# Kernel tuning notes

Measured on AMD Instinct MI355X. Metric: run time of the kernel, lower is better.

Reference implementation:

```python
import jax, jax.numpy as jnp
import numpy as np

N_RAY = 65536
K = 256
NX = NY = NZ = 256


def setup_inputs() -> dict:
    key = jax.random.key(0)
    k1, k2, k3 = jax.random.split(key, 3)
    volume = jax.random.uniform(k1, (NX, NY, NZ), dtype=jnp.float32)
    M = jnp.eye(3, dtype=jnp.float32)          # voxel spacing 1, axis-aligned
    b = jnp.zeros(3, dtype=jnp.float32)        # origin at voxel (0,0,0)
    # rays travel along +z through the volume; random (x, y) entry points
    xy = jax.random.uniform(k2, (N_RAY, 2), minval=0.0, maxval=float(NX - 1), dtype=jnp.float32)
    src = jnp.concatenate([xy, jnp.full((N_RAY, 1), -1.0, dtype=jnp.float32)], axis=1)
    dst = jnp.concatenate([xy, jnp.full((N_RAY, 1), float(NZ), dtype=jnp.float32)], axis=1)
    # sorted sampling parameters t in [0, 1] per ray (uncompressed t_sorted branch)
    t_sorted = jnp.sort(jax.random.uniform(k3, (N_RAY, K), dtype=jnp.float32), axis=1)
    return {"volume": volume, "M": M, "b": b, "src": src, "dst": dst, "t_sorted": t_sorted}


def reference(volume, M, b, src, dst, t_sorted):
    """Faithful jax port of forward_project_3d_torch (uncompressed, fully vectorized)."""
    nx, ny, nz = volume.shape
    M_inv = jnp.linalg.inv(M)
    # sample points along each ray: [N, K, 3]
    direc = (dst - src)[:, None, :]
    pts = src[:, None, :] + t_sorted[:, :, None] * direc
    p0 = pts[:, :-1, :]   # segment starts [N, K-1, 3]
    p1 = pts[:, 1:, :]    # segment ends   [N, K-1, 3]
    inf_mask = jnp.any(jnp.isinf(p0) | jnp.isinf(p1), axis=-1)
    seg_len = jnp.sqrt(jnp.sum((p1 - p0) ** 2, axis=-1))          # [N, K-1]
    mid = 0.5 * (p0 + p1) - b                                      # shifted midpoints
    # voxel-space coordinates: M_inv @ mid, per segment
    ijk_f = jnp.einsum('rc,nkc->nkr', M_inv, mid)                  # [N, K-1, 3]
    ijk = jnp.round(ijk_f).astype(jnp.int32)
    i_idx, j_idx, k_idx = ijk[..., 0], ijk[..., 1], ijk[..., 2]
    oob = (i_idx < 0) | (i_idx >= nx) | (j_idx < 0) | (j_idx >= ny) | (k_idx < 0) | (k_idx >= nz)
    valid = (~inf_mask) & (~oob)
    flat_idx = jnp.where(valid, i_idx * (ny * nz) + j_idx * nz + k_idx, 0)
    vox = volume.reshape(-1)[flat_idx]                             # gather [N, K-1]
    seg_val = jnp.where(valid, vox * seg_len, jnp.zeros_like(seg_len))
    return jnp.sum(seg_val, axis=1)                                # sinogram [N]
```

## Files before the change

kernel.cpp:

```cpp
#include <hip/hip_runtime.h>
#include <math.h>

#define N_RAY 65536
#define KPTS 256
#define NXV 256
#define NYV 256
#define NZV 256
#define RPW 8

typedef float f4vec __attribute__((ext_vector_type(4)));

__global__ __launch_bounds__(256, 4) void ct_proj_kernel(
    const float* __restrict__ volume,
    const float* __restrict__ Mmat,
    const float* __restrict__ bvec,
    const float* __restrict__ src,
    const float* __restrict__ dst,
    const float* __restrict__ t_sorted,
    float* __restrict__ out)
{
    __shared__ float rowbuf[4][2][NZV];

    const int lane = threadIdx.x & 63;
    const int wid  = threadIdx.x >> 6;
    const int wave = blockIdx.x * 4 + wid;
    const int ray0 = wave * RPW;

    float (* __restrict__ slice)[NZV] = rowbuf[wid];

    const int sdi = lane < 24 ? lane : 23;
    const float sv = src[3 * ray0 + sdi];
    const float dv = dst[3 * ray0 + sdi];

    const float* tbase = t_sorted + (size_t)ray0 * KPTS;
    f4vec tvv[RPW];
    #pragma unroll
    for (int i = 0; i < 4; ++i)
        tvv[i] = __builtin_nontemporal_load(
            reinterpret_cast<const f4vec*>(tbase + i * KPTS + 4 * lane));

    const float bx = bvec[0], by = bvec[1], bz = bvec[2];
    const bool fastM =
        (Mmat[0] == 1.0f) && (Mmat[1] == 0.0f) && (Mmat[2] == 0.0f) &&
        (Mmat[3] == 0.0f) && (Mmat[4] == 1.0f) && (Mmat[5] == 0.0f) &&
        (Mmat[6] == 0.0f) && (Mmat[7] == 0.0f) && (Mmat[8] == 1.0f) &&
        (bx == 0.0f) && (by == 0.0f) && (bz == 0.0f);

    unsigned fmask = 0u, imask = 0u;
    unsigned RO[RPW];
    #pragma unroll
    for (int i = 0; i < RPW; ++i) {
        const float sx = __shfl(sv, 3 * i + 0, 64);
        const float sy = __shfl(sv, 3 * i + 1, 64);
        const float sz = __shfl(sv, 3 * i + 2, 64);
        const float dxv = __fsub_rn(__shfl(dv, 3 * i + 0, 64), sx);
        const float dyv = __fsub_rn(__shfl(dv, 3 * i + 1, 64), sy);
        const float dzv = __fsub_rn(__shfl(dv, 3 * i + 2, 64), sz);
        const bool fr = fastM && (dxv == 0.0f) && (dyv == 0.0f) &&
                        isfinite(sx) && isfinite(sy) && isfinite(sz) &&
                        isfinite(dzv);
        const int ii = (int)rintf(sx);
        const int jj = (int)rintf(sy);
        const bool inb = ((unsigned)ii < NXV) && ((unsigned)jj < NYV);
        fmask |= (fr  ? 1u : 0u) << i;
        imask |= (inb ? 1u : 0u) << i;
        RO[i] = __builtin_amdgcn_readfirstlane(
            (fr && inb) ? ((unsigned)ii * NYV + (unsigned)jj) * NZV : 0u);
    }
    fmask = __builtin_amdgcn_readfirstlane(fmask);
    imask = __builtin_amdgcn_readfirstlane(imask);

    const unsigned vo = 4u * (unsigned)lane;
    f4vec rvv[RPW];
    #pragma unroll
    for (int i = 0; i < 3; ++i)
        rvv[i] = *reinterpret_cast<const f4vec*>(volume + RO[i] + vo);

    #define WRITE_SLICE(s, r) do {                 \
        slice[s][0 * 64 + lane] = (r).x;           \
        slice[s][1 * 64 + lane] = (r).y;           \
        slice[s][2 * 64 + lane] = (r).z;           \
        slice[s][3 * 64 + lane] = (r).w;           \
    } while (0)

    WRITE_SLICE(0, rvv[0]);

    #pragma unroll
    for (int i = 0; i < RPW; ++i) {
        if (i + 1 < RPW) WRITE_SLICE((i + 1) & 1, rvv[i + 1]);
        if (i + 3 < RPW)
            rvv[i + 3] = *reinterpret_cast<const f4vec*>(volume + RO[i + 3] + vo);
        if (i + 4 < RPW)
            tvv[i + 4] = __builtin_nontemporal_load(
                reinterpret_cast<const f4vec*>(tbase + (i + 4) * KPTS + 4 * lane));

        const int ray = ray0 + i;
        float acc = 0.0f;

        if ((fmask >> i) & 1u) {
            if ((imask >> i) & 1u) {
                const float sz  = __shfl(sv, 3 * i + 2, 64);
                const float dzv = __fsub_rn(__shfl(dv, 3 * i + 2, 64), sz);
                const f4vec tv  = tvv[i];
                const float t4  = __shfl_down(tv.x, 1, 64);
                const float* __restrict__ buf = slice[i & 1];

                const float p0 = __fadd_rn(sz, __fmul_rn(tv.x, dzv));
                const float p1 = __fadd_rn(sz, __fmul_rn(tv.y, dzv));
                const float p2 = __fadd_rn(sz, __fmul_rn(tv.z, dzv));
                const float p3 = __fadd_rn(sz, __fmul_rn(tv.w, dzv));
                const float p4 = __fadd_rn(sz, __fmul_rn(t4,   dzv));

                const bool f0 = !isinf(p0), f1 = !isinf(p1), f2 = !isinf(p2),
                           f3 = !isinf(p3), f4 = !isinf(p4);

                {
                    const float ez   = __fsub_rn(p1, p0);
                    const float midz = __fmul_rn(0.5f, __fadd_rn(p0, p1));
                    const int   kk   = (int)rintf(midz);
                    const bool  v    = ((unsigned)kk < NZV) && f0 && f1;
                    const int   a    = ((kk & 3) << 6) + (kk >> 2);
                    acc = fmaf(buf[v ? a : 0], v ? fabsf(ez) : 0.0f, acc);
                }
                {
                    const float ez   = __fsub_rn(p2, p1);
                    const float midz = __fmul_rn(0.5f, __fadd_rn(p1, p2));
                    const int   kk   = (int)rintf(midz);
                    const bool  v    = ((unsigned)kk < NZV) && f1 && f2;
                    const int   a    = ((kk & 3) << 6) + (kk >> 2);
                    acc = fmaf(buf[v ? a : 0], v ? fabsf(ez) : 0.0f, acc);
                }
                {
                    const float ez   = __fsub_rn(p3, p2);
                    const float midz = __fmul_rn(0.5f, __fadd_rn(p2, p3));
                    const int   kk   = (int)rintf(midz);
                    const bool  v    = ((unsigned)kk < NZV) && f2 && f3;
                    const int   a    = ((kk & 3) << 6) + (kk >> 2);
                    acc = fmaf(buf[v ? a : 0], v ? fabsf(ez) : 0.0f, acc);
                }
                {
                    const float ez   = __fsub_rn(p4, p3);
                    const float midz = __fmul_rn(0.5f, __fadd_rn(p3, p4));
                    const int   kk   = (int)rintf(midz);
                    const bool  v    = ((unsigned)kk < NZV) && f3 && f4 &&
                                       (lane != 63);
                    const int   a    = ((kk & 3) << 6) + (kk >> 2);
                    acc = fmaf(buf[v ? a : 0], v ? fabsf(ez) : 0.0f, acc);
                }
            }
        } else {
            const float sx = __shfl(sv, 3 * i + 0, 64);
            const float sy = __shfl(sv, 3 * i + 1, 64);
            const float sz = __shfl(sv, 3 * i + 2, 64);
            const float dxv = __fsub_rn(__shfl(dv, 3 * i + 0, 64), sx);
            const float dyv = __fsub_rn(__shfl(dv, 3 * i + 1, 64), sy);
            const float dzv = __fsub_rn(__shfl(dv, 3 * i + 2, 64), sz);

            const float m00 = Mmat[0], m01 = Mmat[1], m02 = Mmat[2];
            const float m10 = Mmat[3], m11 = Mmat[4], m12 = Mmat[5];
            const float m20 = Mmat[6], m21 = Mmat[7], m22 = Mmat[8];
            const float c00 =  (m11 * m22 - m12 * m21);
            const float c01 = -(m10 * m22 - m12 * m20);
            const float c02 =  (m10 * m21 - m11 * m20);
            const float det = m00 * c00 + m01 * c01 + m02 * c02;
            const float id  = 1.0f / det;
            const float i00 = c00 * id;
            const float i01 = -(m01 * m22 - m02 * m21) * id;
            const float i02 =  (m01 * m12 - m02 * m11) * id;
            const float i10 = c01 * id;
            const float i11 =  (m00 * m22 - m02 * m20) * id;
            const float i12 = -(m00 * m12 - m02 * m10) * id;
            const float i20 = c02 * id;
            const float i21 = -(m00 * m21 - m01 * m20) * id;
            const float i22 =  (m00 * m11 - m01 * m10) * id;

            const float* t = tbase + i * KPTS;
            #pragma unroll
            for (int it = 0; it < 4; ++it) {
                const int idx = it * 64 + lane;
                if (idx < KPTS - 1) {
                    const float tkv  = t[idx];
                    const float tk1v = t[idx + 1];
                    const float p0x = __fadd_rn(sx, __fmul_rn(tkv,  dxv));
                    const float p0y = __fadd_rn(sy, __fmul_rn(tkv,  dyv));
                    const float p0z = __fadd_rn(sz, __fmul_rn(tkv,  dzv));
                    const float p1x = __fadd_rn(sx, __fmul_rn(tk1v, dxv));
                    const float p1y = __fadd_rn(sy, __fmul_rn(tk1v, dyv));
                    const float p1z = __fadd_rn(sz, __fmul_rn(tk1v, dzv));

                    const bool infm = isinf(p0x) || isinf(p0y) || isinf(p0z) ||
                                      isinf(p1x) || isinf(p1y) || isinf(p1z);

                    const float ex = __fsub_rn(p1x, p0x);
                    const float ey = __fsub_rn(p1y, p0y);
                    const float ez = __fsub_rn(p1z, p0z);
                    const float seg = sqrtf(ex * ex + ey * ey + ez * ez);

                    const float mx = __fsub_rn(__fmul_rn(0.5f, __fadd_rn(p0x, p1x)), bx);
                    const float my = __fsub_rn(__fmul_rn(0.5f, __fadd_rn(p0y, p1y)), by);
                    const float mz = __fsub_rn(__fmul_rn(0.5f, __fadd_rn(p0z, p1z)), bz);

                    const float fi = __fadd_rn(__fadd_rn(__fmul_rn(i00, mx), __fmul_rn(i01, my)), __fmul_rn(i02, mz));
                    const float fj = __fadd_rn(__fadd_rn(__fmul_rn(i10, mx), __fmul_rn(i11, my)), __fmul_rn(i12, mz));
                    const float fk = __fadd_rn(__fadd_rn(__fmul_rn(i20, mx), __fmul_rn(i21, my)), __fmul_rn(i22, mz));

                    const int ii = (int)rintf(fi);
                    const int jj = (int)rintf(fj);
                    const int kk = (int)rintf(fk);

                    const bool oob = (ii < 0) || (ii >= NXV) ||
                                     (jj < 0) || (jj >= NYV) ||
                                     (kk < 0) || (kk >= NZV);

                    if (!infm && !oob) {
                        const float vox = volume[((size_t)ii * NYV + jj) * NZV + kk];
                        acc = fmaf(vox, seg, acc);
                    }
                }
            }
        }

        #pragma unroll
        for (int off = 32; off >= 1; off >>= 1)
            acc += __shfl_xor(acc, off, 64);

        if (lane == 0) out[ray] = acc;
    }
    #undef WRITE_SLICE
}

extern "C" void kernel_launch(void* const* d_in, const int* in_sizes, int n_in,
                              void* d_out, int out_size, void* d_ws, size_t ws_size,
                              hipStream_t stream) {
    const float* volume   = (const float*)d_in[0];
    const float* Mmat     = (const float*)d_in[1];
    const float* bvec     = (const float*)d_in[2];
    const float* src      = (const float*)d_in[3];
    const float* dst      = (const float*)d_in[4];
    const float* t_sorted = (const float*)d_in[5];
    float* out = (float*)d_out;

    const int grid = N_RAY / (RPW * 4);
    ct_proj_kernel<<<grid, 256, 0, stream>>>(volume, Mmat, bvec, src, dst,
                                             t_sorted, out);
}
```

Measured before the change: 152.5 us.

## Stream t-values and volume rows into LDS via global_load_lds with a 4-slot pipeline

Replaces register-held prefetches plus manual LDS writes with direct global-to-LDS DMA loads (global_load_lds) for both the t_sorted rows and the volume z-rows. A 4-slot ring per wave keeps three rays in flight, synchronised with explicit vmcnt/lgkmcnt waits. It also drops the swizzled LDS layout in favour of linear indexing, writes all 8 ray outputs with one coalesced store, and hoists the M inverse out of the slow-path loop. The intent is to cut VGPR pressure and LDS write instructions and to improve latency hiding. The cost is reliance on hand-tuned waitcnt counts, removal of the min-occupancy launch bound, and possible LDS bank conflicts from the linear layout.

```diff
diff --git a/kernel.cpp b/kernel.cpp
--- a/kernel.cpp
+++ b/kernel.cpp
@@ -10,7 +10,15 @@
 
 typedef float f4vec __attribute__((ext_vector_type(4)));
 
-__global__ __launch_bounds__(256, 4) void ct_proj_kernel(
+#define GLDS16(gsrc, ldst)                                                \
+    __builtin_amdgcn_global_load_lds(                                     \
+        (const __attribute__((address_space(1))) void*)(gsrc),            \
+        (__attribute__((address_space(3))) void*)(ldst), 16, 0, 0)
+
+#define WAITVM(n)  asm volatile("s_waitcnt vmcnt(" #n ")" ::: "memory")
+#define WAITLGKM0  asm volatile("s_waitcnt lgkmcnt(0)" ::: "memory")
+
+__global__ __launch_bounds__(256) void ct_proj_kernel(
     const float* __restrict__ volume,
     const float* __restrict__ Mmat,
     const float* __restrict__ bvec,
@@ -19,25 +27,16 @@
     const float* __restrict__ t_sorted,
     float* __restrict__ out)
 {
-    __shared__ float rowbuf[4][2][NZV];
+    __shared__ float tslot[4][4][KPTS];
+    __shared__ float rslot[4][4][NZV];
 
     const int lane = threadIdx.x & 63;
     const int wid  = threadIdx.x >> 6;
-    const int wave = blockIdx.x * 4 + wid;
-    const int ray0 = wave * RPW;
-
-    float (* __restrict__ slice)[NZV] = rowbuf[wid];
+    const int ray0 = (blockIdx.x * 4 + wid) * RPW;
 
     const int sdi = lane < 24 ? lane : 23;
     const float sv = src[3 * ray0 + sdi];
     const float dv = dst[3 * ray0 + sdi];
-
-    const float* tbase = t_sorted + (size_t)ray0 * KPTS;
-    f4vec tvv[RPW];
-    #pragma unroll
-    for (int i = 0; i < 4; ++i)
-        tvv[i] = __builtin_nontemporal_load(
-            reinterpret_cast<const f4vec*>(tbase + i * KPTS + 4 * lane));
 
     const float bx = bvec[0], by = bvec[1], bz = bvec[2];
     const bool fastM =
@@ -70,85 +69,110 @@
     fmask = __builtin_amdgcn_readfirstlane(fmask);
     imask = __builtin_amdgcn_readfirstlane(imask);
 
-    const unsigned vo = 4u * (unsigned)lane;
-    f4vec rvv[RPW];
-    #pragma unroll
-    for (int i = 0; i < 3; ++i)
-        rvv[i] = *reinterpret_cast<const f4vec*>(volume + RO[i] + vo);
-
-    #define WRITE_SLICE(s, r) do {                 \
-        slice[s][0 * 64 + lane] = (r).x;           \
-        slice[s][1 * 64 + lane] = (r).y;           \
-        slice[s][2 * 64 + lane] = (r).z;           \
-        slice[s][3 * 64 + lane] = (r).w;           \
-    } while (0)
-
-    WRITE_SLICE(0, rvv[0]);
-
-    #pragma unroll
-    for (int i = 0; i < RPW; ++i) {
-        if (i + 1 < RPW) WRITE_SLICE((i + 1) & 1, rvv[i + 1]);
-        if (i + 3 < RPW)
-            rvv[i + 3] = *reinterpret_cast<const f4vec*>(volume + RO[i + 3] + vo);
-        if (i + 4 < RPW)
-            tvv[i + 4] = __builtin_nontemporal_load(
-                reinterpret_cast<const f4vec*>(tbase + (i + 4) * KPTS + 4 * lane));
-
-        const int ray = ray0 + i;
-        float acc = 0.0f;
-
-        if ((fmask >> i) & 1u) {
-            if ((imask >> i) & 1u) {
-                const float sz  = __shfl(sv, 3 * i + 2, 64);
-                const float dzv = __fsub_rn(__shfl(dv, 3 * i + 2, 64), sz);
-                const f4vec tv  = tvv[i];
-                const float t4  = __shfl_down(tv.x, 1, 64);
-                const float* __restrict__ buf = slice[i & 1];
-
-                const float p0 = __fadd_rn(sz, __fmul_rn(tv.x, dzv));
-                const float p1 = __fadd_rn(sz, __fmul_rn(tv.y, dzv));
-                const float p2 = __fadd_rn(sz, __fmul_rn(tv.z, dzv));
-                const float p3 = __fadd_rn(sz, __fmul_rn(tv.w, dzv));
-                const float p4 = __fadd_rn(sz, __fmul_rn(t4,   dzv));
-
-                const bool f0 = !isinf(p0), f1 = !isinf(p1), f2 = !isinf(p2),
-                           f3 = !isinf(p3), f4 = !isinf(p4);
-
-                {
-                    const float ez   = __fsub_rn(p1, p0);
-                    const float midz = __fmul_rn(0.5f, __fadd_rn(p0, p1));
-                    const int   kk   = (int)rintf(midz);
-                    const bool  v    = ((unsigned)kk < NZV) && f0 && f1;
-                    const int   a    = ((kk & 3) << 6) + (kk >> 2);
-                    acc = fmaf(buf[v ? a : 0], v ? fabsf(ez) : 0.0f, acc);
-                }
-                {
-                    const float ez   = __fsub_rn(p2, p1);
-                    const float midz = __fmul_rn(0.5f, __fadd_rn(p1, p2));
-                    const int   kk   = (int)rintf(midz);
-                    const bool  v    = ((unsigned)kk < NZV) && f1 && f2;
-                    const int   a    = ((kk & 3) << 6) + (kk >> 2);
-                    acc = fmaf(buf[v ? a : 0], v ? fabsf(ez) : 0.0f, acc);
-                }
-                {
-                    const float ez   = __fsub_rn(p3, p2);
-                    const float midz = __fmul_rn(0.5f, __fadd_rn(p2, p3));
-                    const int   kk   = (int)rintf(midz);
-                    const bool  v    = ((unsigned)kk < NZV) && f2 && f3;
-                    const int   a    = ((kk & 3) << 6) + (kk >> 2);
-                    acc = fmaf(buf[v ? a : 0], v ? fabsf(ez) : 0.0f, acc);
-                }
-                {
-                    const float ez   = __fsub_rn(p4, p3);
-                    const float midz = __fmul_rn(0.5f, __fadd_rn(p3, p4));
-                    const int   kk   = (int)rintf(midz);
-                    const bool  v    = ((unsigned)kk < NZV) && f3 && f4 &&
-                                       (lane != 63);
-                    const int   a    = ((kk & 3) << 6) + (kk >> 2);
-                    acc = fmaf(buf[v ? a : 0], v ? fabsf(ez) : 0.0f, acc);
-                }
-            }
-        } else {
+    const float* tbase = t_sorted + (size_t)ray0 * KPTS;
+    float rsel = 0.0f;
+
+    if (fmask == 0xFFu) {
+        WAITVM(0);
+
+        #pragma unroll
+        for (int i = 0; i < 3; ++i) {
+            GLDS16(tbase + i * KPTS + 4 * lane, &tslot[wid][i][0]);
+            GLDS16(volume + RO[i] + 4 * lane,   &rslot[wid][i][0]);
+        }
+
+        #pragma unroll
+        for (int i = 0; i < RPW; ++i) {
+            if (i < 5) {
+                WAITLGKM0;
+                GLDS16(tbase + (i + 3) * KPTS + 4 * lane,
+                       &tslot[wid][(i + 3) & 3][0]);
+                GLDS16(volume + RO[i + 3] + 4 * lane,
+                       &rslot[wid][(i + 3) & 3][0]);
+            }
+            if (i <= 4)      { WAITVM(6); }
+            else if (i == 5) { WAITVM(4); }
+            else if (i == 6) { WAITVM(2); }
+            else             { WAITVM(0); }
+
+            const float* __restrict__ tb = &tslot[wid][i & 3][0];
+            const float* __restrict__ rb = &rslot[wid][i & 3][0];
+
+            const f4vec tv = *reinterpret_cast<const f4vec*>(tb + 4 * lane);
+            const float t4 = __shfl_down(tv.x, 1, 64);
+
+            const float sz  = __shfl(sv, 3 * i + 2, 64);
+            const float dzv = __fsub_rn(__shfl(dv, 3 * i + 2, 64), sz);
+            const bool  inb = (imask >> i) & 1u;
+
+            const float p0 = __fadd_rn(sz, __fmul_rn(tv.x, dzv));
+            const float p1 = __fadd_rn(sz, __fmul_rn(tv.y, dzv));
+            const float p2 = __fadd_rn(sz, __fmul_rn(tv.z, dzv));
+            const float p3 = __fadd_rn(sz, __fmul_rn(tv.w, dzv));
+            const float p4 = __fadd_rn(sz, __fmul_rn(t4,   dzv));
+
+            const bool f0 = !isinf(p0), f1 = !isinf(p1), f2 = !isinf(p2),
+                       f3 = !isinf(p3), f4 = !isinf(p4);
+
+            float acc = 0.0f;
+            {
+                const float ez   = __fsub_rn(p1, p0);
+                const float midz = __fmul_rn(0.5f, __fadd_rn(p0, p1));
+                const int   kk   = (int)rintf(midz);
+                const bool  v    = ((unsigned)kk < NZV) && f0 && f1 && inb;
+                acc = fmaf(rb[v ? kk : 0], v ? fabsf(ez) : 0.0f, acc);
+            }
+            {
+                const float ez   = __fsub_rn(p2, p1);
+                const float midz = __fmul_rn(0.5f, __fadd_rn(p1, p2));
+                const int   kk   = (int)rintf(midz);
+                const bool  v    = ((unsigned)kk < NZV) && f1 && f2 && inb;
+                acc = fmaf(rb[v ? kk : 0], v ? fabsf(ez) : 0.0f, acc);
+            }
+            {
+                const float ez   = __fsub_rn(p3, p2);
+                const float midz = __fmul_rn(0.5f, __fadd_rn(p2, p3));
+                const int   kk   = (int)rintf(midz);
+                const bool  v    = ((unsigned)kk < NZV) && f2 && f3 && inb;
+                acc = fmaf(rb[v ? kk : 0], v ? fabsf(ez) : 0.0f, acc);
+            }
+            {
+                const float ez   = __fsub_rn(p4, p3);
+                const float midz = __fmul_rn(0.5f, __fadd_rn(p3, p4));
+                const int   kk   = (int)rintf(midz);
+                const bool  v    = ((unsigned)kk < NZV) && f3 && f4 && inb &&
+                                   (lane != 63);
+                acc = fmaf(rb[v ? kk : 0], v ? fabsf(ez) : 0.0f, acc);
+            }
+
+            #pragma unroll
+            for (int off = 32; off >= 1; off >>= 1)
+                acc += __shfl_xor(acc, off, 64);
+
+            rsel = (lane == i) ? acc : rsel;
+        }
+
+        if (lane < RPW) out[ray0 + lane] = rsel;
+    } else {
+        const float m00 = Mmat[0], m01 = Mmat[1], m02 = Mmat[2];
+        const float m10 = Mmat[3], m11 = Mmat[4], m12 = Mmat[5];
+        const float m20 = Mmat[6], m21 = Mmat[7], m22 = Mmat[8];
+        const float c00 =  (m11 * m22 - m12 * m21);
+        const float c01 = -(m10 * m22 - m12 * m20);
+        const float c02 =  (m10 * m21 - m11 * m20);
+        const float det = m00 * c00 + m01 * c01 + m02 * c02;
+        const float id  = 1.0f / det;
+        const float i00 = c00 * id;
+        const float i01 = -(m01 * m22 - m02 * m21) * id;
+        const float i02 =  (m01 * m12 - m02 * m11) * id;
+        const float i10 = c01 * id;
+        const float i11 =  (m00 * m22 - m02 * m20) * id;
+        const float i12 = -(m00 * m12 - m02 * m10) * id;
+        const float i20 = c02 * id;
+        const float i21 = -(m00 * m21 - m01 * m20) * id;
+        const float i22 =  (m00 * m11 - m01 * m10) * id;
+
+        for (int i = 0; i < RPW; ++i) {
             const float sx = __shfl(sv, 3 * i + 0, 64);
             const float sy = __shfl(sv, 3 * i + 1, 64);
             const float sz = __shfl(sv, 3 * i + 2, 64);
@@ -156,25 +180,8 @@
             const float dyv = __fsub_rn(__shfl(dv, 3 * i + 1, 64), sy);
             const float dzv = __fsub_rn(__shfl(dv, 3 * i + 2, 64), sz);
 
-            const float m00 = Mmat[0], m01 = Mmat[1], m02 = Mmat[2];
-            const float m10 = Mmat[3], m11 = Mmat[4], m12 = Mmat[5];
-            const float m20 = Mmat[6], m21 = Mmat[7], m22 = Mmat[8];
-            const float c00 =  (m11 * m22 - m12 * m21);
-            const float c01 = -(m10 * m22 - m12 * m20);
-            const float c02 =  (m10 * m21 - m11 * m20);
-            const float det = m00 * c00 + m01 * c01 + m02 * c02;
-            const float id  = 1.0f / det;
-            const float i00 = c00 * id;
-            const float i01 = -(m01 * m22 - m02 * m21) * id;
-            const float i02 =  (m01 * m12 - m02 * m11) * id;
-            const float i10 = c01 * id;
-            const float i11 =  (m00 * m22 - m02 * m20) * id;
-            const float i12 = -(m00 * m12 - m02 * m10) * id;
-            const float i20 = c02 * id;
-            const float i21 = -(m00 * m21 - m01 * m20) * id;
-            const float i22 =  (m00 * m11 - m01 * m10) * id;
-
             const float* t = tbase + i * KPTS;
+            float acc = 0.0f;
             #pragma unroll
             for (int it = 0; it < 4; ++it) {
                 const int idx = it * 64 + lane;
@@ -218,15 +225,12 @@
                     }
                 }
             }
+            #pragma unroll
+            for (int off = 32; off >= 1; off >>= 1)
+                acc += __shfl_xor(acc, off, 64);
+            if (lane == 0) out[ray0 + i] = acc;
         }
-
-        #pragma unroll
-        for (int off = 32; off >= 1; off >>= 1)
-            acc += __shfl_xor(acc, off, 64);
-
-        if (lane == 0) out[ray] = acc;
     }
-    #undef WRITE_SLICE
 }
 
 extern "C" void kernel_launch(void* const* d_in, const int* in_sizes, int n_in,
```

Result: faster. 148.0 us (-2.9%).
